# Kernel optimization log

Measured on AMD Instinct MI355X. Metric: run time of the kernel, lower is better.

The kernel has to match this reference:

```python
import jax, jax.numpy as jnp
import numpy as np

BETA = 0.9
THR = 1.0
ALPHA = 2.0  # snntorch surrogate.atan default

@jax.custom_vjp
def atan_spike(x):
    return (x > 0).astype(x.dtype)

def _atan_fwd(x):
    return atan_spike(x), x

def _atan_bwd(x, g):
    # snntorch ATan surrogate: alpha/2 / (1 + (pi/2 * alpha * x)^2)
    return (g * (ALPHA / 2.0) / (1.0 + (jnp.pi / 2.0 * ALPHA * x) ** 2),)

atan_spike.defvjp(_atan_fwd, _atan_bwd)

def setup_inputs() -> dict:
    key = jax.random.key(0)
    k = jax.random.split(key, 5)
    B, T, C, H, W = 128, 25, 3, 64, 64
    F, HID, O = C * H * W, 2048, 2
    bound1 = 1.0 / np.sqrt(F)
    boundo = 1.0 / np.sqrt(HID)
    return {
        "x": jax.random.normal(k[0], (B, T, C, H, W), jnp.float32),
        "W1": jax.random.uniform(k[1], (HID, F), jnp.float32, -bound1, bound1),
        "b1": jax.random.uniform(k[2], (HID,), jnp.float32, -bound1, bound1),
        "Wo": jax.random.uniform(k[3], (O, HID), jnp.float32, -boundo, boundo),
        "bo": jax.random.uniform(k[4], (O,), jnp.float32, -boundo, boundo),
    }

def reference(x, W1, b1, Wo, bo):
    B, T = x.shape[0], x.shape[1]
    HID, O = W1.shape[0], Wo.shape[0]
    xf = x.reshape(B, T, -1).transpose(1, 0, 2)  # [T, B, F]
    # fc1 for all timesteps at once (input is fixed per step)
    h_all = jnp.einsum('tbf,hf->tbh', xf, W1) + b1  # [T, B, HID]

    def step(carry, h):
        mem1, memo = carry
        # snntorch Leaky (reset_mechanism='subtract'): reset from previous mem
        r1 = atan_spike(mem1 - THR)
        mem1 = BETA * mem1 + h - r1 * THR
        s1 = atan_spike(mem1 - THR)
        o = s1 @ Wo.T + bo
        ro = atan_spike(memo - THR)
        memo = BETA * memo + o - ro * THR
        so = atan_spike(memo - THR)
        return (mem1, memo), so

    init = (jnp.zeros((B, HID), x.dtype), jnp.zeros((B, O), x.dtype))
    (_, _), spk_rec = jax.lax.scan(step, init, h_all)
    # train=False path: sum of output spikes over time
    return spk_rec.sum(axis=0)  # [B, O]
```

## Files before the change

kernel.cpp:

```cpp
#include <hip/hip_runtime.h>


#define T_STEPS 25
#define B_SZ    128
#define F_SZ    12288
#define HID_SZ  2048
#define KT      384
#define KT2     192
#define A_CH    32768
#define B_CH    32768
#define M_PAD   3328

typedef __attribute__((ext_vector_type(8))) _Float16 f16x8;
typedef __attribute__((ext_vector_type(4))) float f32x4;

__device__ __forceinline__ void g2l16(const void* g, void* l) {
  __builtin_amdgcn_global_load_lds(
      (const __attribute__((address_space(1))) void*)g,
      (__attribute__((address_space(3))) void*)l, 16, 0, 0);
}

__global__ __launch_bounds__(256) void conv_x_kernel(
    const float* __restrict__ x, char* __restrict__ A2) {
  const int total = 13 * KT * 256 * 4;
  for (int i = blockIdx.x * 256 + threadIdx.x; i < total; i += gridDim.x * 256) {
    const int s = i & 3;
    const int r = (i >> 2) & 255;
    const int rest = i >> 10;
    const int ks = rest % KT;
    const int mt = rest / KT;
    const int m = mt * 256 + r;
    const int b = m & 127;
    const int t = m >> 7;
    f16x8 hi = {0, 0, 0, 0, 0, 0, 0, 0};
    f16x8 lo = {0, 0, 0, 0, 0, 0, 0, 0};
    if (t < T_STEPS) {
      const float* src = x + ((size_t)(b * T_STEPS + t)) * F_SZ + ks * 32 + s * 8;
      float4 v0 = *(const float4*)src;
      float4 v1 = *(const float4*)(src + 4);
      float vf[8] = {v0.x, v0.y, v0.z, v0.w, v1.x, v1.y, v1.z, v1.w};
#pragma unroll
      for (int j = 0; j < 8; ++j) {
        _Float16 h = (_Float16)vf[j];
        hi[j] = h;
        lo[j] = (_Float16)(vf[j] - (float)h);
      }
    }
    char* chunk = A2 + (size_t)rest * A_CH;
    *(f16x8*)(chunk + s * 4096 + r * 16) = hi;
    *(f16x8*)(chunk + (s + 4) * 4096 + r * 16) = lo;
  }
}

__global__ __launch_bounds__(256) void conv_w_kernel(
    const float* __restrict__ W1, char* __restrict__ B2) {
  const int total = 8 * KT * 256 * 4;
  for (int i = blockIdx.x * 256 + threadIdx.x; i < total; i += gridDim.x * 256) {
    const int s = i & 3;
    const int r = (i >> 2) & 255;
    const int rest = i >> 10;
    const int ks = rest % KT;
    const int nt = rest / KT;
    const float* src = W1 + ((size_t)(nt * 256 + r)) * F_SZ + ks * 32 + s * 8;
    float4 v0 = *(const float4*)src;
    float4 v1 = *(const float4*)(src + 4);
    float vf[8] = {v0.x, v0.y, v0.z, v0.w, v1.x, v1.y, v1.z, v1.w};
    f16x8 hi, lo;
#pragma unroll
    for (int j = 0; j < 8; ++j) {
      float vs = vf[j] * 128.0f;
      _Float16 h = (_Float16)vs;
      hi[j] = h;
      lo[j] = (_Float16)(vs - (float)h);
    }
    char* chunk = B2 + (size_t)rest * B_CH;
    *(f16x8*)(chunk + s * 4096 + r * 16) = hi;
    *(f16x8*)(chunk + (s + 4) * 4096 + r * 16) = lo;
  }
}

__global__ __launch_bounds__(512, 2) void gemm_mfma_kernel(
    const char* __restrict__ A2, const char* __restrict__ B2,
    float* __restrict__ parts) {
  __shared__ __align__(16) char lds[131072];
  const int tid = threadIdx.x;
  const int l = tid & 63;
  const int w = tid >> 6;
  const int wm = w >> 2;
  const int wn = w & 3;

  const int bid = blockIdx.x;
  const int swz = (bid & 7) * 26 + (bid >> 3);
  const int mt = swz >> 4;
  const int nt = (swz >> 1) & 7;
  const int sp = swz & 1;
  const char* aSrc = A2 + (size_t)(mt * KT + sp * KT2) * A_CH;
  const char* bSrc = B2 + (size_t)(nt * KT + sp * KT2) * B_CH;

#define STAGE(ktx)                                                         \
  do {                                                                     \
    const char* sa_ = aSrc + (size_t)(ktx) * A_CH + tid * 16;              \
    const char* sb_ = bSrc + (size_t)(ktx) * B_CH + tid * 16;              \
    char* da_ = (char*)lds + ((ktx) & 1) * 65536 + w * 1024;               \
    char* db_ = da_ + 32768;                                               \
    g2l16(sa_, da_);                 g2l16(sa_ + 8192, da_ + 8192);        \
    g2l16(sa_ + 16384, da_ + 16384); g2l16(sa_ + 24576, da_ + 24576);     \
    g2l16(sb_, db_);                 g2l16(sb_ + 8192, db_ + 8192);        \
    g2l16(sb_ + 16384, db_ + 16384); g2l16(sb_ + 24576, db_ + 24576);     \
  } while (0)

  f32x4 acc[8][4];
#pragma unroll
  for (int i = 0; i < 8; ++i)
#pragma unroll
    for (int j = 0; j < 4; ++j) acc[i][j] = (f32x4){0.f, 0.f, 0.f, 0.f};

  const int aoff = (l >> 4) * 4096 + (wm * 128 + (l & 15)) * 16;
  const int boff = (l >> 4) * 4096 + (wn * 64 + (l & 15)) * 16;

#define MM3(mf, nf, AH, AL, BH, BL)                                                      \
  acc[mf][nf] = __builtin_amdgcn_mfma_f32_16x16x32_f16(AH, BH, acc[mf][nf], 0, 0, 0);    \
  acc[mf][nf] = __builtin_amdgcn_mfma_f32_16x16x32_f16(AH, BL, acc[mf][nf], 0, 0, 0);    \
  acc[mf][nf] = __builtin_amdgcn_mfma_f32_16x16x32_f16(AL, BH, acc[mf][nf], 0, 0, 0);

  STAGE(0);

  for (int kt = 0; kt < KT2; ++kt) {
    __syncthreads();
    if (kt + 1 < KT2) STAGE(kt + 1);

    const char* la = (const char*)lds + (kt & 1) * 65536;
    const char* lb = la + 32768;

    f16x8 ah[8], al[8];
#pragma unroll
    for (int mf = 0; mf < 8; ++mf) {
      ah[mf] = *(const f16x8*)(la + aoff + mf * 256);
      al[mf] = *(const f16x8*)(la + aoff + 16384 + mf * 256);
    }
#pragma unroll
    for (int nf = 0; nf < 4; ++nf) {
      f16x8 bh = *(const f16x8*)(lb + boff + nf * 256);
      f16x8 bl = *(const f16x8*)(lb + boff + 16384 + nf * 256);
      __builtin_amdgcn_s_setprio(1);
      MM3(0, nf, ah[0], al[0], bh, bl)
      MM3(1, nf, ah[1], al[1], bh, bl)
      MM3(2, nf, ah[2], al[2], bh, bl)
      MM3(3, nf, ah[3], al[3], bh, bl)
      MM3(4, nf, ah[4], al[4], bh, bl)
      MM3(5, nf, ah[5], al[5], bh, bl)
      MM3(6, nf, ah[6], al[6], bh, bl)
      MM3(7, nf, ah[7], al[7], bh, bl)
      __builtin_amdgcn_s_setprio(0);
    }
  }

  float* dst = parts + (size_t)sp * ((size_t)M_PAD * HID_SZ);
  const int row0 = mt * 256 + wm * 128 + (l >> 4) * 4;
  const int col0 = nt * 256 + wn * 64 + (l & 15);
#pragma unroll
  for (int nf = 0; nf < 4; ++nf) {
    const int col = col0 + nf * 16;
#pragma unroll
    for (int mf = 0; mf < 8; ++mf) {
#pragma unroll
      for (int q = 0; q < 4; ++q) {
        const int row = row0 + mf * 16 + q;
        dst[(size_t)row * HID_SZ + col] = acc[mf][nf][q];
      }
    }
  }
#undef STAGE
#undef MM3
}

__global__ __launch_bounds__(256) void gemm_h_kernel(
    const float* __restrict__ x, const float* __restrict__ W1,
    const float* __restrict__ b1, float* __restrict__ h_all) {
  __shared__ float As[16][128];
  __shared__ float Bs[16][128];
  const int tid = threadIdx.x;
  const int tx = tid & 15;
  const int ty = tid >> 4;
  const int m0 = blockIdx.x * 128;
  const int n0 = blockIdx.y * 128;
  const int lrow = tid >> 1;
  const int lcol = (tid & 1) * 8;
  const int gm = m0 + lrow;
  const int bb = gm & (B_SZ - 1);
  const int tt = gm >> 7;
  const float* aptr = x + ((size_t)bb * T_STEPS + tt) * F_SZ + lcol;
  const float* bptr = W1 + (size_t)(n0 + lrow) * F_SZ + lcol;
  float acc[8][8];
#pragma unroll
  for (int i = 0; i < 8; ++i)
#pragma unroll
    for (int j = 0; j < 8; ++j) acc[i][j] = 0.f;
  for (int k0 = 0; k0 < F_SZ; k0 += 16) {
    float4 av0 = *(const float4*)(aptr + k0);
    float4 av1 = *(const float4*)(aptr + k0 + 4);
    float4 bv0 = *(const float4*)(bptr + k0);
    float4 bv1 = *(const float4*)(bptr + k0 + 4);
    As[lcol + 0][lrow] = av0.x; As[lcol + 1][lrow] = av0.y;
    As[lcol + 2][lrow] = av0.z; As[lcol + 3][lrow] = av0.w;
    As[lcol + 4][lrow] = av1.x; As[lcol + 5][lrow] = av1.y;
    As[lcol + 6][lrow] = av1.z; As[lcol + 7][lrow] = av1.w;
    Bs[lcol + 0][lrow] = bv0.x; Bs[lcol + 1][lrow] = bv0.y;
    Bs[lcol + 2][lrow] = bv0.z; Bs[lcol + 3][lrow] = bv0.w;
    Bs[lcol + 4][lrow] = bv1.x; Bs[lcol + 5][lrow] = bv1.y;
    Bs[lcol + 6][lrow] = bv1.z; Bs[lcol + 7][lrow] = bv1.w;
    __syncthreads();
#pragma unroll
    for (int k = 0; k < 16; ++k) {
      float4 a0 = *(const float4*)&As[k][ty * 8];
      float4 a1 = *(const float4*)&As[k][ty * 8 + 4];
      float4 q0 = *(const float4*)&Bs[k][tx * 8];
      float4 q1 = *(const float4*)&Bs[k][tx * 8 + 4];
      float ar[8] = {a0.x, a0.y, a0.z, a0.w, a1.x, a1.y, a1.z, a1.w};
      float br[8] = {q0.x, q0.y, q0.z, q0.w, q1.x, q1.y, q1.z, q1.w};
#pragma unroll
      for (int i = 0; i < 8; ++i)
#pragma unroll
        for (int j = 0; j < 8; ++j)
          acc[i][j] = fmaf(ar[i], br[j], acc[i][j]);
    }
    __syncthreads();
  }
#pragma unroll
  for (int i = 0; i < 8; ++i) {
    const int gm2 = m0 + ty * 8 + i;
    float* orow = h_all + (size_t)gm2 * HID_SZ + n0 + tx * 8;
    const float* brow = b1 + n0 + tx * 8;
#pragma unroll
    for (int j = 0; j < 8; ++j) orow[j] = acc[i][j] + brow[j];
  }
}

__global__ __launch_bounds__(256) void lif_scan_kernel(
    const float* __restrict__ p0, const float* __restrict__ p1,
    const float* __restrict__ b1, const float* __restrict__ Wo,
    const float* __restrict__ bo, float* __restrict__ out, int two_parts) {
  const int b = blockIdx.x;
  const int tid = threadIdx.x;
  float mem1[8];
  float wo0[8], wo1[8], bv[8];
#pragma unroll
  for (int i = 0; i < 8; ++i) {
    mem1[i] = 0.f;
    wo0[i] = Wo[tid + 256 * i];
    wo1[i] = Wo[HID_SZ + tid + 256 * i];
    bv[i] = b1[tid + 256 * i];
  }
  __shared__ float partial[4][2];
  float memo0 = 0.f, memo1 = 0.f, acc0 = 0.f, acc1 = 0.f;
  const float bo0 = bo[0], bo1 = bo[1];
  for (int t = 0; t < T_STEPS; ++t) {
    const size_t rowb = ((size_t)t * B_SZ + b) * HID_SZ;
    float p0v = 0.f, p1v = 0.f;
    float pr0 = 0.f, pr1 = 0.f;
#pragma unroll
    for (int i = 0; i < 8; ++i) {
      const size_t idx = rowb + tid + 256 * i;
      float h;
      if (two_parts)
        h = (p0[idx] + p1[idx]) * 0.0078125f + bv[i];
      else
        h = p0[idx];
      float r1 = mem1[i] > 1.0f ? 1.0f : 0.0f;
      float m = 0.9f * mem1[i] + h - r1;
      mem1[i] = m;
      if (m > 1.0f) { pr0 += wo0[i]; pr1 += wo1[i]; }
    }
#pragma unroll
    for (int off = 32; off > 0; off >>= 1) {
      pr0 += __shfl_down(pr0, off);
      pr1 += __shfl_down(pr1, off);
    }
    const int wave = tid >> 6;
    if ((tid & 63) == 0) { partial[wave][0] = pr0; partial[wave][1] = pr1; }
    __syncthreads();
    if (tid == 0) {
      float o0 = partial[0][0] + partial[1][0] + partial[2][0] + partial[3][0] + bo0;
      float o1 = partial[0][1] + partial[1][1] + partial[2][1] + partial[3][1] + bo1;
      float ro0 = memo0 > 1.0f ? 1.0f : 0.0f;
      float ro1 = memo1 > 1.0f ? 1.0f : 0.0f;
      memo0 = 0.9f * memo0 + o0 - ro0;
      memo1 = 0.9f * memo1 + o1 - ro1;
      acc0 += memo0 > 1.0f ? 1.0f : 0.0f;
      acc1 += memo1 > 1.0f ? 1.0f : 0.0f;
    }
    __syncthreads();
    (void)p0v; (void)p1v;
  }
  if (tid == 0) {
    out[b * 2 + 0] = acc0;
    out[b * 2 + 1] = acc1;
  }
}

extern "C" void kernel_launch(void* const* d_in, const int* in_sizes, int n_in,
                              void* d_out, int out_size, void* d_ws, size_t ws_size,
                              hipStream_t stream) {
  const float* x  = (const float*)d_in[0];
  const float* W1 = (const float*)d_in[1];
  const float* b1 = (const float*)d_in[2];
  const float* Wo = (const float*)d_in[3];
  const float* bo = (const float*)d_in[4];
  float* out = (float*)d_out;

  const size_t part_bytes = (size_t)M_PAD * HID_SZ * 4;
  const size_t a2_bytes = (size_t)13 * KT * A_CH;
  const size_t b2_bytes = (size_t)8 * KT * B_CH;
  char* ws = (char*)d_ws;
  float* parts = (float*)ws;

  if (ws_size >= 2 * part_bytes + a2_bytes + b2_bytes) {
    char* A2 = ws + 2 * part_bytes;
    char* B2 = A2 + a2_bytes;
    conv_x_kernel<<<2048, 256, 0, stream>>>(x, A2);
    conv_w_kernel<<<2048, 256, 0, stream>>>(W1, B2);
    gemm_mfma_kernel<<<208, 512, 0, stream>>>(A2, B2, parts);
    lif_scan_kernel<<<B_SZ, 256, 0, stream>>>(
        parts, parts + (size_t)M_PAD * HID_SZ, b1, Wo, bo, out, 1);
  } else {
    dim3 grid(25, 16);
    gemm_h_kernel<<<grid, 256, 0, stream>>>(x, W1, b1, (float*)ws);
    lif_scan_kernel<<<B_SZ, 256, 0, stream>>>(
        (const float*)ws, (const float*)ws, b1, Wo, bo, out, 0);
  }
}
```

Measured before the change: 555.0 us.

## Add Stream-K style persistent GEMM splitting K work evenly across 256 blocks

```diff
diff --git a/kernel.cpp b/kernel.cpp
--- a/kernel.cpp
+++ b/kernel.cpp
@@ -10,6 +10,8 @@
 #define A_CH    32768
 #define B_CH    32768
 #define M_PAD   3328
+#define UPB     156
+#define PART_STRIDE ((size_t)M_PAD * HID_SZ)
 
 typedef __attribute__((ext_vector_type(8))) _Float16 f16x8;
 typedef __attribute__((ext_vector_type(4))) float f32x4;
@@ -79,24 +81,6 @@
   }
 }
 
-__global__ __launch_bounds__(512, 2) void gemm_mfma_kernel(
-    const char* __restrict__ A2, const char* __restrict__ B2,
-    float* __restrict__ parts) {
-  __shared__ __align__(16) char lds[131072];
-  const int tid = threadIdx.x;
-  const int l = tid & 63;
-  const int w = tid >> 6;
-  const int wm = w >> 2;
-  const int wn = w & 3;
-
-  const int bid = blockIdx.x;
-  const int swz = (bid & 7) * 26 + (bid >> 3);
-  const int mt = swz >> 4;
-  const int nt = (swz >> 1) & 7;
-  const int sp = swz & 1;
-  const char* aSrc = A2 + (size_t)(mt * KT + sp * KT2) * A_CH;
-  const char* bSrc = B2 + (size_t)(nt * KT + sp * KT2) * B_CH;
-
 #define STAGE(ktx)                                                         \
   do {                                                                     \
     const char* sa_ = aSrc + (size_t)(ktx) * A_CH + tid * 16;              \
@@ -109,29 +93,131 @@
     g2l16(sb_ + 16384, db_ + 16384); g2l16(sb_ + 24576, db_ + 24576);     \
   } while (0)
 
-  f32x4 acc[8][4];
-#pragma unroll
-  for (int i = 0; i < 8; ++i)
-#pragma unroll
-    for (int j = 0; j < 4; ++j) acc[i][j] = (f32x4){0.f, 0.f, 0.f, 0.f};
-
-  const int aoff = (l >> 4) * 4096 + (wm * 128 + (l & 15)) * 16;
-  const int boff = (l >> 4) * 4096 + (wn * 64 + (l & 15)) * 16;
-
 #define MM3(mf, nf, AH, AL, BH, BL)                                                      \
   acc[mf][nf] = __builtin_amdgcn_mfma_f32_16x16x32_f16(AH, BH, acc[mf][nf], 0, 0, 0);    \
   acc[mf][nf] = __builtin_amdgcn_mfma_f32_16x16x32_f16(AH, BL, acc[mf][nf], 0, 0, 0);    \
   acc[mf][nf] = __builtin_amdgcn_mfma_f32_16x16x32_f16(AL, BH, acc[mf][nf], 0, 0, 0);
 
+__global__ __launch_bounds__(512, 2) void gemm_persist_kernel(
+    const char* __restrict__ A2, const char* __restrict__ B2,
+    float* __restrict__ parts) {
+  __shared__ __align__(16) char lds[131072];
+  const int tid = threadIdx.x;
+  const int l = tid & 63;
+  const int w = tid >> 6;
+  const int wm = w >> 2;
+  const int wn = w & 3;
+
+  const int bid = blockIdx.x;
+  const int swz = (bid & 7) * 32 + (bid >> 3);
+
+  const int aoff = (l >> 4) * 4096 + (wm * 128 + (l & 15)) * 16;
+  const int boff = (l >> 4) * 4096 + (wn * 64 + (l & 15)) * 16;
+
+  int u = swz * UPB;
+  const int u1 = u + UPB;
+
+  while (u < u1) {
+    const int mnt = u / 384;
+    const int kt0 = u - mnt * 384;
+    const int seg = min(384 - kt0, u1 - u);
+    const int ktN = kt0 + seg;
+    const int mt = mnt >> 3;
+    const int nt = mnt & 7;
+    const char* aSrc = A2 + (size_t)mt * KT * A_CH;
+    const char* bSrc = B2 + (size_t)nt * KT * B_CH;
+
+    f32x4 acc[8][4];
+#pragma unroll
+    for (int i = 0; i < 8; ++i)
+#pragma unroll
+      for (int j = 0; j < 4; ++j) acc[i][j] = (f32x4){0.f, 0.f, 0.f, 0.f};
+
+    STAGE(kt0);
+
+    for (int kt = kt0; kt < ktN; ++kt) {
+      __syncthreads();
+      if (kt + 1 < ktN) STAGE(kt + 1);
+
+      const char* la = (const char*)lds + (kt & 1) * 65536;
+      const char* lb = la + 32768;
+
+      f16x8 ah[8], al[8];
+#pragma unroll
+      for (int mf = 0; mf < 8; ++mf) {
+        ah[mf] = *(const f16x8*)(la + aoff + mf * 256);
+        al[mf] = *(const f16x8*)(la + aoff + 16384 + mf * 256);
+      }
+#pragma unroll
+      for (int nf = 0; nf < 4; ++nf) {
+        f16x8 bh = *(const f16x8*)(lb + boff + nf * 256);
+        f16x8 bl = *(const f16x8*)(lb + boff + 16384 + nf * 256);
+        __builtin_amdgcn_s_setprio(1);
+        MM3(0, nf, ah[0], al[0], bh, bl)
+        MM3(1, nf, ah[1], al[1], bh, bl)
+        MM3(2, nf, ah[2], al[2], bh, bl)
+        MM3(3, nf, ah[3], al[3], bh, bl)
+        MM3(4, nf, ah[4], al[4], bh, bl)
+        MM3(5, nf, ah[5], al[5], bh, bl)
+        MM3(6, nf, ah[6], al[6], bh, bl)
+        MM3(7, nf, ah[7], al[7], bh, bl)
+        __builtin_amdgcn_s_setprio(0);
+      }
+    }
+
+    const int slot = swz - (mnt * 384) / UPB;
+    float* dst = parts + (size_t)slot * PART_STRIDE;
+    const int row0 = mt * 256 + wm * 128 + (l >> 4) * 4;
+    const int col0 = nt * 256 + wn * 64 + (l & 15);
+#pragma unroll
+    for (int nf = 0; nf < 4; ++nf) {
+      const int col = col0 + nf * 16;
+#pragma unroll
+      for (int mf = 0; mf < 8; ++mf) {
+#pragma unroll
+        for (int q = 0; q < 4; ++q) {
+          const int row = row0 + mf * 16 + q;
+          dst[(size_t)row * HID_SZ + col] = acc[mf][nf][q];
+        }
+      }
+    }
+    u += seg;
+    __syncthreads();
+  }
+}
+
+__global__ __launch_bounds__(512, 2) void gemm_mfma_kernel(
+    const char* __restrict__ A2, const char* __restrict__ B2,
+    float* __restrict__ parts) {
+  __shared__ __align__(16) char lds[131072];
+  const int tid = threadIdx.x;
+  const int l = tid & 63;
+  const int w = tid >> 6;
+  const int wm = w >> 2;
+  const int wn = w & 3;
+  const int bid = blockIdx.x;
+  const int swz = (bid & 7) * 26 + (bid >> 3);
+  const int mt = swz >> 4;
+  const int nt = (swz >> 1) & 7;
+  const int sp = swz & 1;
+  const char* aSrc = A2 + (size_t)(mt * KT + sp * KT2) * A_CH;
+  const char* bSrc = B2 + (size_t)(nt * KT + sp * KT2) * B_CH;
+
+  f32x4 acc[8][4];
+#pragma unroll
+  for (int i = 0; i < 8; ++i)
+#pragma unroll
+    for (int j = 0; j < 4; ++j) acc[i][j] = (f32x4){0.f, 0.f, 0.f, 0.f};
+
+  const int aoff = (l >> 4) * 4096 + (wm * 128 + (l & 15)) * 16;
+  const int boff = (l >> 4) * 4096 + (wn * 64 + (l & 15)) * 16;
+
   STAGE(0);
-
   for (int kt = 0; kt < KT2; ++kt) {
     __syncthreads();
     if (kt + 1 < KT2) STAGE(kt + 1);
-
     const char* la = (const char*)lds + (kt & 1) * 65536;
     const char* lb = la + 32768;
-
     f16x8 ah[8], al[8];
 #pragma unroll
     for (int mf = 0; mf < 8; ++mf) {
@@ -154,8 +240,7 @@
       __builtin_amdgcn_s_setprio(0);
     }
   }
-
-  float* dst = parts + (size_t)sp * ((size_t)M_PAD * HID_SZ);
+  float* dst = parts + (size_t)sp * PART_STRIDE;
   const int row0 = mt * 256 + wm * 128 + (l >> 4) * 4;
   const int col0 = nt * 256 + wn * 64 + (l & 15);
 #pragma unroll
@@ -170,8 +255,6 @@
       }
     }
   }
-#undef STAGE
-#undef MM3
 }
 
 __global__ __launch_bounds__(256) void gemm_h_kernel(
@@ -237,9 +320,9 @@
 }
 
 __global__ __launch_bounds__(256) void lif_scan_kernel(
-    const float* __restrict__ p0, const float* __restrict__ p1,
-    const float* __restrict__ b1, const float* __restrict__ Wo,
-    const float* __restrict__ bo, float* __restrict__ out, int two_parts) {
+    const float* __restrict__ parts, const float* __restrict__ b1,
+    const float* __restrict__ Wo, const float* __restrict__ bo,
+    float* __restrict__ out, int mode) {
   const int b = blockIdx.x;
   const int tid = threadIdx.x;
   float mem1[8];
@@ -255,17 +338,27 @@
   float memo0 = 0.f, memo1 = 0.f, acc0 = 0.f, acc1 = 0.f;
   const float bo0 = bo[0], bo1 = bo[1];
   for (int t = 0; t < T_STEPS; ++t) {
-    const size_t rowb = ((size_t)t * B_SZ + b) * HID_SZ;
-    float p0v = 0.f, p1v = 0.f;
+    const int row = t * B_SZ + b;
+    const size_t rowb = (size_t)row * HID_SZ;
+    const int mt = row >> 8;
     float pr0 = 0.f, pr1 = 0.f;
 #pragma unroll
     for (int i = 0; i < 8; ++i) {
       const size_t idx = rowb + tid + 256 * i;
       float h;
-      if (two_parts)
-        h = (p0[idx] + p1[idx]) * 0.0078125f + bv[i];
-      else
-        h = p0[idx];
+      if (mode == 2) {
+        const int mnt = mt * 8 + i;
+        const int k0 = mnt * 384;
+        const int ns = (k0 + 383) / UPB - k0 / UPB + 1;
+        float s = parts[idx] + parts[idx + PART_STRIDE] +
+                  parts[idx + 2 * PART_STRIDE];
+        if (ns == 4) s += parts[idx + 3 * PART_STRIDE];
+        h = s * 0.0078125f + bv[i];
+      } else if (mode == 1) {
+        h = (parts[idx] + parts[idx + PART_STRIDE]) * 0.0078125f + bv[i];
+      } else {
+        h = parts[idx];
+      }
       float r1 = mem1[i] > 1.0f ? 1.0f : 0.0f;
       float m = 0.9f * mem1[i] + h - r1;
       mem1[i] = m;
@@ -290,7 +383,6 @@
       acc1 += memo1 > 1.0f ? 1.0f : 0.0f;
     }
     __syncthreads();
-    (void)p0v; (void)p1v;
   }
   if (tid == 0) {
     out[b * 2 + 0] = acc0;
@@ -308,24 +400,30 @@
   const float* bo = (const float*)d_in[4];
   float* out = (float*)d_out;
 
-  const size_t part_bytes = (size_t)M_PAD * HID_SZ * 4;
+  const size_t part_bytes = PART_STRIDE * 4;
   const size_t a2_bytes = (size_t)13 * KT * A_CH;
   const size_t b2_bytes = (size_t)8 * KT * B_CH;
   char* ws = (char*)d_ws;
   float* parts = (float*)ws;
 
-  if (ws_size >= 2 * part_bytes + a2_bytes + b2_bytes) {
+  if (ws_size >= 4 * part_bytes + a2_bytes + b2_bytes) {
+    char* A2 = ws + 4 * part_bytes;
+    char* B2 = A2 + a2_bytes;
+    conv_x_kernel<<<2048, 256, 0, stream>>>(x, A2);
+    conv_w_kernel<<<2048, 256, 0, stream>>>(W1, B2);
+    gemm_persist_kernel<<<256, 512, 0, stream>>>(A2, B2, parts);
+    lif_scan_kernel<<<B_SZ, 256, 0, stream>>>(parts, b1, Wo, bo, out, 2);
+  } else if (ws_size >= 2 * part_bytes + a2_bytes + b2_bytes) {
     char* A2 = ws + 2 * part_bytes;
     char* B2 = A2 + a2_bytes;
     conv_x_kernel<<<2048, 256, 0, stream>>>(x, A2);
     conv_w_kernel<<<2048, 256, 0, stream>>>(W1, B2);
     gemm_mfma_kernel<<<208, 512, 0, stream>>>(A2, B2, parts);
-    lif_scan_kernel<<<B_SZ, 256, 0, stream>>>(
-        parts, parts + (size_t)M_PAD * HID_SZ, b1, Wo, bo, out, 1);
+    lif_scan_kernel<<<B_SZ, 256, 0, stream>>>(parts, b1, Wo, bo, out, 1);
   } else {
     dim3 grid(25, 16);
     gemm_h_kernel<<<grid, 256, 0, stream>>>(x, W1, b1, (float*)ws);
     lif_scan_kernel<<<B_SZ, 256, 0, stream>>>(
-        (const float*)ws, (const float*)ws, b1, Wo, bo, out, 0);
-  }
-}
+        (const float*)ws, b1, Wo, bo, out, 0);
+  }
+}
```

Result: slower. 609.7 us (+9.9%).
